# Kernel optimization log

Measured on AMD Instinct MI355X. Metric: run time of the kernel, lower is better.

The kernel has to match this reference:

```python
import jax, jax.numpy as jnp
import numpy as np


def setup_inputs() -> dict:
    key = jax.random.key(0)
    ks = jax.random.split(key, 10)
    N, D, B, K, Ppool, Dout = 100000, 128, 8192, 64, 2048, 128
    return {
        "features": jax.random.normal(ks[0], (N, D), dtype=jnp.float32),
        "all_logits": jax.random.normal(ks[1], (N, 2), dtype=jnp.float32),
        "center_logits": jax.random.normal(ks[2], (B, 2), dtype=jnp.float32),
        "train_pos_logits": jax.random.normal(ks[3], (Ppool, 2), dtype=jnp.float32),
        "W": jax.random.normal(ks[4], (Dout, 2 * D), dtype=jnp.float32) * 0.05,
        "b": jax.random.normal(ks[5], (Dout,), dtype=jnp.float32) * 0.05,
        "center_idx": jax.random.randint(ks[6], (B,), 0, N),
        "neighbor_idx": jax.random.randint(ks[7], (B, K), 0, N),
        "train_pos_idx": jax.random.randint(ks[8], (Ppool,), 0, N),
        "labels": jax.random.randint(ks[9], (B,), 0, 2),
        "avg_half_pos_neigh": 32,
    }


def reference(features, all_logits, center_logits, train_pos_logits, W, b,
              center_idx, neighbor_idx, train_pos_idx, labels, avg_half_pos_neigh):
    B, K = neighbor_idx.shape
    S = K // 2 + 1                      # closest half of neighbors (+1)
    P = avg_half_pos_neigh + 1          # extra same-class (positive) picks
    # distance on class-0 logit between each center and its neighbors: [B, K]
    nb_logit0 = all_logits[neighbor_idx, 0]
    d = jnp.abs(nb_logit0 - center_logits[:, :1])
    # select S smallest distances (argsort()[:S] equivalent)
    _, sel = jax.lax.top_k(-d, S)                       # [B, S]
    sel_nodes = jnp.take_along_axis(neighbor_idx, sel, axis=1)  # [B, S]
    nb_sum = features[sel_nodes].sum(axis=1)            # [B, D]
    # positive-label augmentation: P closest train-positive nodes
    d2 = jnp.abs(train_pos_logits[None, :, 0] - center_logits[:, :1])  # [B, Ppool]
    _, sel2 = jax.lax.top_k(-d2, P)                     # [B, P]
    minor_sum = features[train_pos_idx[sel2]].sum(axis=1)  # [B, D]
    is_pos = (labels == 1).astype(features.dtype)[:, None]
    agg = (nb_sum + is_pos * minor_sum) / (S + is_pos * P)
    cat = jnp.concatenate([features[center_idx], agg], axis=1)  # [B, 2D]
    return jax.nn.relu(cat @ W.T + b)
```

## Files before the change

### kernel.cpp

```cpp
#include <hip/hip_runtime.h>


__global__ __launch_bounds__(256) void sort_pool_kernel(
    const float* __restrict__ tp_logits,
    const int*   __restrict__ tp_idx,
    float* __restrict__ sv,
    int*   __restrict__ sg,
    int Ppool)
{
    __shared__ float v[2048];
    const int t = threadIdx.x;
    const float2* tp2 = (const float2*)tp_logits;
    const bool useL = (Ppool <= 2048);
    if (useL) {
        for (int j = t; j < Ppool; j += 256) v[j] = tp2[j].x;
        __syncthreads();
    }
    const int lane = t & 63;
    const int i = blockIdx.x * 4 + (t >> 6);
    if (i >= Ppool) return;
    const float vi = useL ? v[i] : tp2[i].x;
    int r = 0;
    for (int j = lane; j < Ppool; j += 64) {
        float vj = useL ? v[j] : tp2[j].x;
        r += (int)((vj < vi) | ((vj == vi) & (j < i)));
    }
#pragma unroll
    for (int off = 32; off > 0; off >>= 1) r += __shfl_down(r, off);
    if (lane == 0) { sv[r] = vi; sg[r] = tp_idx[i]; }
}

__global__ __launch_bounds__(256) void row_kernel(
    const float* __restrict__ features,
    const float* __restrict__ all_logits,
    const float* __restrict__ center_logits,
    const int*   __restrict__ center_idx,
    const int*   __restrict__ neighbor_idx,
    const int*   __restrict__ labels,
    const int*   __restrict__ avgp,
    const float* __restrict__ sv,
    const int*   __restrict__ sg,
    float* __restrict__ cat,
    int K, int S, int Ppool, int D)
{
    __shared__ int    sel[96];
    __shared__ float  wd[96];
    __shared__ float4 red4[4][32];
    __shared__ int    lo_s;

    const int b    = blockIdx.x;
    const int t    = threadIdx.x;
    const int lane = t & 63;
    const int wave = t >> 6;
    const float c0 = center_logits[2 * b];
    const int isPos = (labels[b] == 1);
    const int P = isPos ? (avgp[0] + 1) : 0;
    const int nf4 = D >> 2;
    const float4* f4 = (const float4*)features;
    float4* cat4 = (float4*)cat;
    const size_t cb4 = (size_t)b * (size_t)(2 * nf4);

    if (wave == 0) {
        float dv = 3.4e38f;
        int nb = 0;
        if (lane < K) {
            nb = neighbor_idx[(size_t)b * K + lane];
            dv = fabsf(all_logits[2 * nb] - c0);
        }
        int r = 0;
#pragma unroll
        for (int j = 0; j < 64; ++j) {
            float dj = __shfl(dv, j);
            r += (int)((dj < dv) | ((dj == dv) & (j < lane)));
        }
        if (lane < K && r < S) sel[r] = nb;
    } else if (wave == 1) {
        if (isPos) {
            int cnt = 0;
            for (int j = lane; j < Ppool; j += 64) cnt += (int)(sv[j] < c0);
#pragma unroll
            for (int off = 32; off > 0; off >>= 1) cnt += __shfl_down(cnt, off);
            if (lane == 0) lo_s = cnt;
        }
    } else if (wave == 2) {
        if (lane < nf4)
            cat4[cb4 + lane] = f4[(size_t)center_idx[b] * nf4 + lane];
    }
    __syncthreads();

    int w0 = 0, wsz = 0;
    if (isPos) {
        const int lo = lo_s;
        w0 = lo - P; if (w0 < 0) w0 = 0;
        int w1 = lo + P; if (w1 > Ppool) w1 = Ppool;
        wsz = w1 - w0;
        if (t < wsz) wd[t] = fabsf(sv[w0 + t] - c0);
    }
    __syncthreads();
    if (isPos && t < wsz) {
        float dvi = wd[t];
        int r = 0;
#pragma unroll 8
        for (int j = 0; j < wsz; ++j) {
            float dj = wd[j];
            r += (int)((dj < dvi) | ((dj == dvi) & (j < t)));
        }
        if (r < P) sel[S + r] = sg[w0 + t];
    }
    __syncthreads();

    const int total = S + P;
    const int g = t >> 5, c = t & 31;
    float4 acc = make_float4(0.f, 0.f, 0.f, 0.f);
    int i = g;
    if (i + 56 < total) {
        float4 x0 = f4[(size_t)sel[i     ] * nf4 + c];
        float4 x1 = f4[(size_t)sel[i +  8] * nf4 + c];
        float4 x2 = f4[(size_t)sel[i + 16] * nf4 + c];
        float4 x3 = f4[(size_t)sel[i + 24] * nf4 + c];
        float4 x4 = f4[(size_t)sel[i + 32] * nf4 + c];
        float4 x5 = f4[(size_t)sel[i + 40] * nf4 + c];
        float4 x6 = f4[(size_t)sel[i + 48] * nf4 + c];
        float4 x7 = f4[(size_t)sel[i + 56] * nf4 + c];
        acc.x = ((x0.x + x1.x) + (x2.x + x3.x)) + ((x4.x + x5.x) + (x6.x + x7.x));
        acc.y = ((x0.y + x1.y) + (x2.y + x3.y)) + ((x4.y + x5.y) + (x6.y + x7.y));
        acc.z = ((x0.z + x1.z) + (x2.z + x3.z)) + ((x4.z + x5.z) + (x6.z + x7.z));
        acc.w = ((x0.w + x1.w) + (x2.w + x3.w)) + ((x4.w + x5.w) + (x6.w + x7.w));
        i += 64;
    }
    if (i + 24 < total) {
        float4 x0 = f4[(size_t)sel[i     ] * nf4 + c];
        float4 x1 = f4[(size_t)sel[i +  8] * nf4 + c];
        float4 x2 = f4[(size_t)sel[i + 16] * nf4 + c];
        float4 x3 = f4[(size_t)sel[i + 24] * nf4 + c];
        acc.x += (x0.x + x1.x) + (x2.x + x3.x);
        acc.y += (x0.y + x1.y) + (x2.y + x3.y);
        acc.z += (x0.z + x1.z) + (x2.z + x3.z);
        acc.w += (x0.w + x1.w) + (x2.w + x3.w);
        i += 32;
    }
    if (i + 8 < total) {
        float4 x0 = f4[(size_t)sel[i    ] * nf4 + c];
        float4 x1 = f4[(size_t)sel[i + 8] * nf4 + c];
        acc.x += x0.x + x1.x; acc.y += x0.y + x1.y;
        acc.z += x0.z + x1.z; acc.w += x0.w + x1.w;
        i += 16;
    }
    for (; i < total; i += 8) {
        float4 x = f4[(size_t)sel[i] * nf4 + c];
        acc.x += x.x; acc.y += x.y; acc.z += x.z; acc.w += x.w;
    }

    float4 o;
    o.x = __shfl_xor(acc.x, 32); o.y = __shfl_xor(acc.y, 32);
    o.z = __shfl_xor(acc.z, 32); o.w = __shfl_xor(acc.w, 32);
    acc.x += o.x; acc.y += o.y; acc.z += o.z; acc.w += o.w;
    if (lane < 32) red4[wave][c] = acc;
    __syncthreads();
    if (t < 32) {
        float4 a0 = red4[0][t], a1 = red4[1][t], a2 = red4[2][t], a3 = red4[3][t];
        float inv = 1.f / (float)total;
        float4 w;
        w.x = (a0.x + a1.x + a2.x + a3.x) * inv;
        w.y = (a0.y + a1.y + a2.y + a3.y) * inv;
        w.z = (a0.z + a1.z + a2.z + a3.z) * inv;
        w.w = (a0.w + a1.w + a2.w + a3.w) * inv;
        cat4[cb4 + nf4 + t] = w;
    }
}

__global__ __launch_bounds__(256) void gemm_relu_kernel(
    const float* __restrict__ A,
    const float* __restrict__ W,
    const float* __restrict__ bias,
    float* __restrict__ out,
    int M, int Kd)
{
    __shared__ __align__(16) float As[32][68];
    __shared__ __align__(16) float Ws[64][132];
    const int t  = threadIdx.x;
    const int m0 = blockIdx.x * 32;
    const int cg = t & 31;
    const int rg = t >> 5;
    float acc[4][4] = {};

    for (int kc = 0; kc < Kd; kc += 64) {
        for (int e = t; e < 512; e += 256) {
            int r = e >> 4, c4 = (e & 15) * 4;
            float4 val = make_float4(0.f, 0.f, 0.f, 0.f);
            int m = m0 + r;
            if (m < M) val = *(const float4*)&A[(size_t)m * Kd + kc + c4];
            *(float4*)&As[r][c4] = val;
        }
        for (int e = t; e < 2048; e += 256) {
            int o = e >> 4, k4 = (e & 15) * 4;
            float4 wv = *(const float4*)&W[(size_t)o * Kd + kc + k4];
            Ws[k4 + 0][o] = wv.x;
            Ws[k4 + 1][o] = wv.y;
            Ws[k4 + 2][o] = wv.z;
            Ws[k4 + 3][o] = wv.w;
        }
        __syncthreads();

        for (int k4 = 0; k4 < 64; k4 += 4) {
            float4 a[4], w[4];
#pragma unroll
            for (int i = 0; i < 4; ++i) a[i] = *(const float4*)&As[rg * 4 + i][k4];
#pragma unroll
            for (int kk = 0; kk < 4; ++kk) w[kk] = *(const float4*)&Ws[k4 + kk][cg * 4];
#pragma unroll
            for (int kk = 0; kk < 4; ++kk) {
#pragma unroll
                for (int i = 0; i < 4; ++i) {
                    float av = ((const float*)&a[i])[kk];
                    acc[i][0] = fmaf(av, w[kk].x, acc[i][0]);
                    acc[i][1] = fmaf(av, w[kk].y, acc[i][1]);
                    acc[i][2] = fmaf(av, w[kk].z, acc[i][2]);
                    acc[i][3] = fmaf(av, w[kk].w, acc[i][3]);
                }
            }
        }
        __syncthreads();
    }

    float4 bv = *(const float4*)&bias[cg * 4];
#pragma unroll
    for (int i = 0; i < 4; ++i) {
        int m = m0 + rg * 4 + i;
        if (m < M) {
            float4 o;
            o.x = fmaxf(acc[i][0] + bv.x, 0.f);
            o.y = fmaxf(acc[i][1] + bv.y, 0.f);
            o.z = fmaxf(acc[i][2] + bv.z, 0.f);
            o.w = fmaxf(acc[i][3] + bv.w, 0.f);
            *(float4*)&out[(size_t)m * 128 + cg * 4] = o;
        }
    }
}

extern "C" void kernel_launch(void* const* d_in, const int* in_sizes, int n_in,
                              void* d_out, int out_size, void* d_ws, size_t ws_size,
                              hipStream_t stream) {
    const float* features      = (const float*)d_in[0];
    const float* all_logits    = (const float*)d_in[1];
    const float* center_logits = (const float*)d_in[2];
    const float* tp_logits     = (const float*)d_in[3];
    const float* W             = (const float*)d_in[4];
    const float* bias          = (const float*)d_in[5];
    const int*   center_idx    = (const int*)d_in[6];
    const int*   neighbor_idx  = (const int*)d_in[7];
    const int*   tp_idx        = (const int*)d_in[8];
    const int*   labels        = (const int*)d_in[9];
    const int*   avgp          = (const int*)d_in[10];

    const int B     = in_sizes[6];
    const int K     = in_sizes[7] / B;
    const int S     = K / 2 + 1;
    const int Ppool = in_sizes[8];
    const int Dout  = in_sizes[5];
    const int D     = in_sizes[4] / (2 * Dout);

    char* ws = (char*)d_ws;
    float* cat  = (float*)ws;
    size_t cat_bytes = (size_t)B * 2 * D * sizeof(float);
    float* sv_g = (float*)(ws + cat_bytes);
    int*   sg_g = (int*)(ws + cat_bytes + (size_t)Ppool * 4);

    sort_pool_kernel<<<(Ppool + 3) / 4, 256, 0, stream>>>(
        tp_logits, tp_idx, sv_g, sg_g, Ppool);

    row_kernel<<<B, 256, 0, stream>>>(
        features, all_logits, center_logits, center_idx, neighbor_idx,
        labels, avgp, sv_g, sg_g, cat, K, S, Ppool, D);

    gemm_relu_kernel<<<(B + 31) / 32, 256, 0, stream>>>(
        cat, W, bias, (float*)d_out, B, 2 * D);
}
```

Measured before the change: 164.4 us.

## Map one wave per batch row in row_kernel instead of one block per row

The row kernel now processes four batch rows per block, one 64-lane wavefront each. Each wave independently does the neighbor rank-select, the pool window select, and the feature gather with float2 loads. This removes the block-wide __syncthreads and shared reductions. It also lets each wave issue up to 16 independent gathers in flight. In exchange, each row runs serially within one wave, including the pool count scan over 2048 entries, so per-row latency grows while the number of blocks drops by four times.

```diff
diff --git a/kernel.cpp b/kernel.cpp
--- a/kernel.cpp
+++ b/kernel.cpp
@@ -41,131 +41,93 @@
     const float* __restrict__ sv,
     const int*   __restrict__ sg,
     float* __restrict__ cat,
-    int K, int S, int Ppool, int D)
+    int K, int S, int Ppool, int D, int B)
 {
-    __shared__ int    sel[96];
-    __shared__ float  wd[96];
-    __shared__ float4 red4[4][32];
-    __shared__ int    lo_s;
-
-    const int b    = blockIdx.x;
+    __shared__ int   sel[4][96];
+    __shared__ float wd[4][96];
+
     const int t    = threadIdx.x;
     const int lane = t & 63;
     const int wave = t >> 6;
-    const float c0 = center_logits[2 * b];
+    const int b    = blockIdx.x * 4 + wave;
+    if (b >= B) return;
+
+    const float c0  = center_logits[2 * b];
     const int isPos = (labels[b] == 1);
-    const int P = isPos ? (avgp[0] + 1) : 0;
-    const int nf4 = D >> 2;
-    const float4* f4 = (const float4*)features;
-    float4* cat4 = (float4*)cat;
-    const size_t cb4 = (size_t)b * (size_t)(2 * nf4);
-
-    if (wave == 0) {
-        float dv = 3.4e38f;
-        int nb = 0;
-        if (lane < K) {
-            nb = neighbor_idx[(size_t)b * K + lane];
-            dv = fabsf(all_logits[2 * nb] - c0);
-        }
-        int r = 0;
-#pragma unroll
-        for (int j = 0; j < 64; ++j) {
-            float dj = __shfl(dv, j);
-            r += (int)((dj < dv) | ((dj == dv) & (j < lane)));
-        }
-        if (lane < K && r < S) sel[r] = nb;
-    } else if (wave == 1) {
-        if (isPos) {
-            int cnt = 0;
-            for (int j = lane; j < Ppool; j += 64) cnt += (int)(sv[j] < c0);
-#pragma unroll
-            for (int off = 32; off > 0; off >>= 1) cnt += __shfl_down(cnt, off);
-            if (lane == 0) lo_s = cnt;
-        }
-    } else if (wave == 2) {
-        if (lane < nf4)
-            cat4[cb4 + lane] = f4[(size_t)center_idx[b] * nf4 + lane];
-    }
-    __syncthreads();
-
-    int w0 = 0, wsz = 0;
+    const int P     = isPos ? (avgp[0] + 1) : 0;
+    const int nf2   = D >> 1;
+    const bool act  = lane < nf2;
+    const float2* f2 = (const float2*)features;
+    float2* cat2 = (float2*)cat;
+    const size_t cb2 = (size_t)b * (size_t)(2 * nf2);
+
+    float2 ctr = make_float2(0.f, 0.f);
+    if (act) ctr = f2[(size_t)center_idx[b] * nf2 + lane];
+
+    float dv = 3.4e38f;
+    int nb = 0;
+    if (lane < K) {
+        nb = neighbor_idx[(size_t)b * K + lane];
+        dv = fabsf(all_logits[2 * nb] - c0);
+    }
+    int r = 0;
+#pragma unroll
+    for (int j = 0; j < 64; ++j) {
+        float dj = __shfl(dv, j);
+        r += (int)((dj < dv) | ((dj == dv) & (j < lane)));
+    }
+    if (lane < K && r < S) sel[wave][r] = nb;
+
     if (isPos) {
-        const int lo = lo_s;
-        w0 = lo - P; if (w0 < 0) w0 = 0;
+        int cnt = 0;
+        for (int j = lane; j < Ppool; j += 64) cnt += (int)(sv[j] < c0);
+#pragma unroll
+        for (int off = 32; off > 0; off >>= 1) cnt += __shfl_down(cnt, off);
+        const int lo = __shfl(cnt, 0);
+        int w0 = lo - P; if (w0 < 0) w0 = 0;
         int w1 = lo + P; if (w1 > Ppool) w1 = Ppool;
-        wsz = w1 - w0;
-        if (t < wsz) wd[t] = fabsf(sv[w0 + t] - c0);
-    }
-    __syncthreads();
-    if (isPos && t < wsz) {
-        float dvi = wd[t];
-        int r = 0;
-#pragma unroll 8
-        for (int j = 0; j < wsz; ++j) {
-            float dj = wd[j];
-            r += (int)((dj < dvi) | ((dj == dvi) & (j < t)));
-        }
-        if (r < P) sel[S + r] = sg[w0 + t];
-    }
-    __syncthreads();
+        const int wsz = w1 - w0;
+        for (int i = lane; i < wsz; i += 64) wd[wave][i] = fabsf(sv[w0 + i] - c0);
+        for (int i = lane; i < wsz; i += 64) {
+            float dvi = wd[wave][i];
+            int rr = 0;
+            for (int j = 0; j < wsz; ++j) {
+                float dj = wd[wave][j];
+                rr += (int)((dj < dvi) | ((dj == dvi) & (j < i)));
+            }
+            if (rr < P) sel[wave][S + rr] = sg[w0 + i];
+        }
+    }
 
     const int total = S + P;
-    const int g = t >> 5, c = t & 31;
-    float4 acc = make_float4(0.f, 0.f, 0.f, 0.f);
-    int i = g;
-    if (i + 56 < total) {
-        float4 x0 = f4[(size_t)sel[i     ] * nf4 + c];
-        float4 x1 = f4[(size_t)sel[i +  8] * nf4 + c];
-        float4 x2 = f4[(size_t)sel[i + 16] * nf4 + c];
-        float4 x3 = f4[(size_t)sel[i + 24] * nf4 + c];
-        float4 x4 = f4[(size_t)sel[i + 32] * nf4 + c];
-        float4 x5 = f4[(size_t)sel[i + 40] * nf4 + c];
-        float4 x6 = f4[(size_t)sel[i + 48] * nf4 + c];
-        float4 x7 = f4[(size_t)sel[i + 56] * nf4 + c];
-        acc.x = ((x0.x + x1.x) + (x2.x + x3.x)) + ((x4.x + x5.x) + (x6.x + x7.x));
-        acc.y = ((x0.y + x1.y) + (x2.y + x3.y)) + ((x4.y + x5.y) + (x6.y + x7.y));
-        acc.z = ((x0.z + x1.z) + (x2.z + x3.z)) + ((x4.z + x5.z) + (x6.z + x7.z));
-        acc.w = ((x0.w + x1.w) + (x2.w + x3.w)) + ((x4.w + x5.w) + (x6.w + x7.w));
-        i += 64;
-    }
-    if (i + 24 < total) {
-        float4 x0 = f4[(size_t)sel[i     ] * nf4 + c];
-        float4 x1 = f4[(size_t)sel[i +  8] * nf4 + c];
-        float4 x2 = f4[(size_t)sel[i + 16] * nf4 + c];
-        float4 x3 = f4[(size_t)sel[i + 24] * nf4 + c];
-        acc.x += (x0.x + x1.x) + (x2.x + x3.x);
-        acc.y += (x0.y + x1.y) + (x2.y + x3.y);
-        acc.z += (x0.z + x1.z) + (x2.z + x3.z);
-        acc.w += (x0.w + x1.w) + (x2.w + x3.w);
-        i += 32;
-    }
-    if (i + 8 < total) {
-        float4 x0 = f4[(size_t)sel[i    ] * nf4 + c];
-        float4 x1 = f4[(size_t)sel[i + 8] * nf4 + c];
-        acc.x += x0.x + x1.x; acc.y += x0.y + x1.y;
-        acc.z += x0.z + x1.z; acc.w += x0.w + x1.w;
-        i += 16;
-    }
-    for (; i < total; i += 8) {
-        float4 x = f4[(size_t)sel[i] * nf4 + c];
-        acc.x += x.x; acc.y += x.y; acc.z += x.z; acc.w += x.w;
-    }
-
-    float4 o;
-    o.x = __shfl_xor(acc.x, 32); o.y = __shfl_xor(acc.y, 32);
-    o.z = __shfl_xor(acc.z, 32); o.w = __shfl_xor(acc.w, 32);
-    acc.x += o.x; acc.y += o.y; acc.z += o.z; acc.w += o.w;
-    if (lane < 32) red4[wave][c] = acc;
-    __syncthreads();
-    if (t < 32) {
-        float4 a0 = red4[0][t], a1 = red4[1][t], a2 = red4[2][t], a3 = red4[3][t];
-        float inv = 1.f / (float)total;
-        float4 w;
-        w.x = (a0.x + a1.x + a2.x + a3.x) * inv;
-        w.y = (a0.y + a1.y + a2.y + a3.y) * inv;
-        w.z = (a0.z + a1.z + a2.z + a3.z) * inv;
-        w.w = (a0.w + a1.w + a2.w + a3.w) * inv;
-        cat4[cb4 + nf4 + t] = w;
+    float2 acc = make_float2(0.f, 0.f);
+    if (act) {
+        int i = 0;
+        while (i + 16 <= total) {
+            float2 x[16];
+#pragma unroll
+            for (int u = 0; u < 16; ++u)
+                x[u] = f2[(size_t)sel[wave][i + u] * nf2 + lane];
+#pragma unroll
+            for (int u = 0; u < 16; ++u) { acc.x += x[u].x; acc.y += x[u].y; }
+            i += 16;
+        }
+        while (i + 4 <= total) {
+            float2 x[4];
+#pragma unroll
+            for (int u = 0; u < 4; ++u)
+                x[u] = f2[(size_t)sel[wave][i + u] * nf2 + lane];
+#pragma unroll
+            for (int u = 0; u < 4; ++u) { acc.x += x[u].x; acc.y += x[u].y; }
+            i += 4;
+        }
+        for (; i < total; ++i) {
+            float2 x = f2[(size_t)sel[wave][i] * nf2 + lane];
+            acc.x += x.x; acc.y += x.y;
+        }
+        const float inv = 1.f / (float)total;
+        cat2[cb2 + lane]       = ctr;
+        cat2[cb2 + nf2 + lane] = make_float2(acc.x * inv, acc.y * inv);
     }
 }
 
@@ -269,9 +231,9 @@
     sort_pool_kernel<<<(Ppool + 3) / 4, 256, 0, stream>>>(
         tp_logits, tp_idx, sv_g, sg_g, Ppool);
 
-    row_kernel<<<B, 256, 0, stream>>>(
+    row_kernel<<<(B + 3) / 4, 256, 0, stream>>>(
         features, all_logits, center_logits, center_idx, neighbor_idx,
-        labels, avgp, sv_g, sg_g, cat, K, S, Ppool, D);
+        labels, avgp, sv_g, sg_g, cat, K, S, Ppool, D, B);
 
     gemm_relu_kernel<<<(B + 31) / 32, 256, 0, stream>>>(
         cat, W, bias, (float*)d_out, B, 2 * D);
```

After: 167.5 us. Within noise of the previous version (+1.8%).
